# Kernel optimization log

Hardware: AMD Instinct MI355X
Metric: run time of the kernel (lower is better)

The kernel has to match this reference:

```python
import jax, jax.numpy as jnp
import numpy as np
from jax import lax

D = 1024      # hidden_dim
H = 1408      # moe_inter_dim
E = 8         # num_experts
K = 2         # topk
ROUTER_SCALE = 1.0


def setup_inputs() -> dict:
    key = jax.random.key(0)
    ks = jax.random.split(key, 16)
    s = 0.02
    inp = {
        "x": jax.random.normal(ks[0], (2, 2048, D), dtype=jnp.float32),
        "gate_w": jax.random.normal(ks[1], (E, D), dtype=jnp.float32) * s,
        "gate_b": jax.random.normal(ks[2], (E,), dtype=jnp.float32) * s,
        # stacked expert params; torch Linear weight [out,in] stored transposed as [in,out]
        "w1": jax.random.normal(ks[3], (E, D, H), dtype=jnp.float32) * s,
        "b1": jax.random.normal(ks[4], (E, H), dtype=jnp.float32) * s,
        "w3": jax.random.normal(ks[5], (E, D, H), dtype=jnp.float32) * s,
        "b3": jax.random.normal(ks[6], (E, H), dtype=jnp.float32) * s,
        "w2": jax.random.normal(ks[7], (E, H, D), dtype=jnp.float32) * s,
        "b2": jax.random.normal(ks[8], (E, D), dtype=jnp.float32) * s,
        # shared expert
        "sw1": jax.random.normal(ks[9], (D, H), dtype=jnp.float32) * s,
        "sb1": jax.random.normal(ks[10], (H,), dtype=jnp.float32) * s,
        "sw3": jax.random.normal(ks[11], (D, H), dtype=jnp.float32) * s,
        "sb3": jax.random.normal(ks[12], (H,), dtype=jnp.float32) * s,
        "sw2": jax.random.normal(ks[13], (H, D), dtype=jnp.float32) * s,
        "sb2": jax.random.normal(ks[14], (D,), dtype=jnp.float32) * s,
    }
    return inp


def _expert(x, w1, b1, w3, b3, w2, b2):
    # NOTE: source applies silu to the PRODUCT: w2(silu(w1(x) * w3(x)))
    h = jax.nn.silu((x @ w1 + b1) * (x @ w3 + b3))
    return h @ w2 + b2


def reference(x, gate_w, gate_b, w1, b1, w3, b3, w2, b2,
              sw1, sb1, sw3, sb3, sw2, sb2):
    shape = x.shape
    xf = x.reshape(-1, D)                      # [T, D]
    T = xf.shape[0]

    # Gate
    scores = jax.nn.softmax(xf @ gate_w.T, axis=-1)   # [T, E]
    biased = scores + gate_b
    _, idx = lax.top_k(biased, K)                     # [T, K] int32
    w = jnp.take_along_axis(scores, idx, axis=-1) * ROUTER_SCALE  # [T, K]

    # Dense routing-weight matrix (top-k indices are distinct per token)
    rw = jnp.zeros((T, E), dtype=xf.dtype).at[jnp.arange(T)[:, None], idx].add(w)

    # Stacked expert compute: [T, E, H] -> [T, E, D], combined by routing weight
    h = jax.nn.silu((jnp.einsum('td,edh->teh', xf, w1) + b1)
                    * (jnp.einsum('td,edh->teh', xf, w3) + b3))
    oe = jnp.einsum('teh,ehd->ted', h, w2) + b2
    y = jnp.einsum('te,ted->td', rw, oe)

    # Shared expert on all tokens
    z = _expert(xf, sw1, sb1, sw3, sb3, sw2, sb2)
    return (y + z).reshape(shape)
```

## Files before the change

kernel.cpp:

```cpp
#include <hip/hip_runtime.h>
#include <math.h>

#define DD 1024
#define HH 1408
#define NE 8

typedef __attribute__((ext_vector_type(8))) __bf16 bf16x8;
typedef __attribute__((ext_vector_type(4))) float f32x4;

__device__ __forceinline__ float bf2f(unsigned short u) {
  union { unsigned int i; float f; } v; v.i = ((unsigned int)u) << 16; return v.f;
}
__device__ __forceinline__ unsigned short f2bf(float f) {
  union { float f; unsigned int i; } v; v.f = f;
  unsigned int r = v.i + 0x7FFFu + ((v.i >> 16) & 1u);
  return (unsigned short)(r >> 16);
}
__device__ __forceinline__ float tof(float f) { return f; }
__device__ __forceinline__ float tof(unsigned short u) { return bf2f(u); }

__device__ __forceinline__ void cvt2(float a, float b, unsigned int* o) {
  asm("v_cvt_pk_bf16_f32 %0, %1, %2" : "=v"(*o) : "v"(a), "v"(b));
}

__device__ __forceinline__ void ld8cvt(const float* p, unsigned int* o) {
  float4 a = *(const float4*)p;
  float4 b = *(const float4*)(p + 4);
  cvt2(a.x, a.y, o + 0); cvt2(a.z, a.w, o + 1);
  cvt2(b.x, b.y, o + 2); cvt2(b.z, b.w, o + 3);
}

typedef unsigned int __attribute__((address_space(1))) gu32;
typedef unsigned int __attribute__((address_space(3))) lu32;
__device__ __forceinline__ void gl16(const unsigned short* g, unsigned short* l) {
  __builtin_amdgcn_global_load_lds((const gu32*)g, (lu32*)l, 16, 0, 0);
}

__global__ void sniff_kernel(const unsigned short* __restrict__ xw,
                             int* __restrict__ dflag) {
  __shared__ int cnt;
  if (threadIdx.x == 0) cnt = 0;
  __syncthreads();
  unsigned short v = xw[threadIdx.x];
  int e = (v >> 7) & 0xFF;
  if (e >= 100 && e <= 140) atomicAdd(&cnt, 1);
  __syncthreads();
  if (threadIdx.x == 0) dflag[0] = (cnt < 230) ? 1 : 0;
}

__global__ void cvtx_kernel(const void* __restrict__ x,
                            const int* __restrict__ dflag,
                            unsigned short* __restrict__ xb, int n8) {
  int i = blockIdx.x * blockDim.x + threadIdx.x;
  int st = gridDim.x * blockDim.x;
  if (dflag[0]) {
    const float* xs = (const float*)x;
    for (; i < n8; i += st) {
      unsigned int o[4];
      ld8cvt(xs + (size_t)i * 8, o);
      *(uint4*)(xb + (size_t)i * 8) = *(uint4*)o;
    }
  } else {
    const uint4* xs = (const uint4*)x;
    for (; i < n8; i += st) *(uint4*)(xb + (size_t)i * 8) = xs[i];
  }
}

__global__ void trans_kernel(const void* __restrict__ wmain,
                             const void* __restrict__ wsh,
                             const int* __restrict__ dflag,
                             unsigned short* __restrict__ out, int R, int C) {
  __shared__ float tile[32][33];
  const int mat = blockIdx.z;
  const int r0 = blockIdx.y << 5, c0 = blockIdx.x << 5;
  const int t = threadIdx.x;
  const int lr = t >> 3, lc = (t & 7) << 2;
  const size_t mbase = (size_t)mat * R * C;
  if (dflag[0]) {
    const float* src = (mat < NE) ? ((const float*)wmain + mbase) : (const float*)wsh;
    float4 v = *(const float4*)(src + (size_t)(r0 + lr) * C + c0 + lc);
    tile[lr][lc] = v.x; tile[lr][lc + 1] = v.y;
    tile[lr][lc + 2] = v.z; tile[lr][lc + 3] = v.w;
  } else {
    const unsigned short* src = (mat < NE) ? ((const unsigned short*)wmain + mbase)
                                           : (const unsigned short*)wsh;
    ushort4 v = *(const ushort4*)(src + (size_t)(r0 + lr) * C + c0 + lc);
    tile[lr][lc] = bf2f(v.x); tile[lr][lc + 1] = bf2f(v.y);
    tile[lr][lc + 2] = bf2f(v.z); tile[lr][lc + 3] = bf2f(v.w);
  }
  __syncthreads();
  const int oc = t >> 3;
  const int orr = (t & 7) << 2;
  unsigned int p0, p1;
  cvt2(tile[orr][oc], tile[orr + 1][oc], &p0);
  cvt2(tile[orr + 2][oc], tile[orr + 3][oc], &p1);
  uint2 pk; pk.x = p0; pk.y = p1;
  *(uint2*)(out + mbase + (size_t)(c0 + oc) * R + r0 + orr) = pk;
}

__global__ void cvtb_kernel(const void* b1, const void* b3, const void* b2,
                            const void* sb1, const void* sb3, const void* sb2,
                            const int* __restrict__ dflag,
                            float* __restrict__ bf1, float* __restrict__ bf3,
                            float* __restrict__ bf2o) {
  int i = blockIdx.x * blockDim.x + threadIdx.x;
  const int nh = (NE + 1) * HH, nd = (NE + 1) * DD;
  const bool f32 = dflag[0] != 0;
  auto get = [&](const void* pm, const void* ps, int idx, int per) -> float {
    int mat = idx / per, j = idx - mat * per;
    if (f32) return (mat < NE) ? ((const float*)pm)[(size_t)mat * per + j]
                               : ((const float*)ps)[j];
    return bf2f((mat < NE) ? ((const unsigned short*)pm)[(size_t)mat * per + j]
                           : ((const unsigned short*)ps)[j]);
  };
  if (i < nh) bf1[i] = get(b1, sb1, i, HH);
  else if (i < 2 * nh) bf3[i - nh] = get(b3, sb3, i - nh, HH);
  else if (i < 2 * nh + nd) bf2o[i - 2 * nh] = get(b2, sb2, i - 2 * nh, DD);
}

template <class T>
__device__ void gate_body(const T* __restrict__ x,
                          const T* __restrict__ gw,
                          const T* __restrict__ gb,
                          int* __restrict__ tok_eidx,
                          float* __restrict__ tok_w, int T_) {
  int t = (int)((blockIdx.x * blockDim.x + threadIdx.x) >> 6);
  int lane = threadIdx.x & 63;
  if (t >= T_) return;
  const T* xr = x + (size_t)t * DD;
  float acc[NE];
#pragma unroll
  for (int e = 0; e < NE; e++) acc[e] = 0.f;
  for (int i = lane; i < DD; i += 64) {
    float xv = tof(xr[i]);
#pragma unroll
    for (int e = 0; e < NE; e++) acc[e] += xv * tof(gw[e * DD + i]);
  }
#pragma unroll
  for (int off = 32; off > 0; off >>= 1) {
#pragma unroll
    for (int e = 0; e < NE; e++) acc[e] += __shfl_xor(acc[e], off);
  }
  if (lane == 0) {
    float mx = acc[0];
#pragma unroll
    for (int e = 1; e < NE; e++) mx = fmaxf(mx, acc[e]);
    float s = 0.f, sc[NE], bi[NE];
#pragma unroll
    for (int e = 0; e < NE; e++) { sc[e] = expf(acc[e] - mx); s += sc[e]; }
    float inv = 1.f / s;
#pragma unroll
    for (int e = 0; e < NE; e++) { sc[e] *= inv; bi[e] = sc[e] + tof(gb[e]); }
    int i1 = 0;
#pragma unroll
    for (int e = 1; e < NE; e++) if (bi[e] > bi[i1]) i1 = e;
    int i2 = (i1 == 0) ? 1 : 0;
#pragma unroll
    for (int e = 0; e < NE; e++) if (e != i1 && bi[e] > bi[i2]) i2 = e;
    tok_eidx[t * 2] = i1; tok_eidx[t * 2 + 1] = i2;
    tok_w[t * 2] = sc[i1]; tok_w[t * 2 + 1] = sc[i2];
  }
}

__global__ void gate_kernel(const void* x, const void* gw, const void* gb,
                            const int* __restrict__ dflag,
                            int* tok_eidx, float* tok_w, int T_) {
  if (dflag[0])
    gate_body<float>((const float*)x, (const float*)gw, (const float*)gb,
                     tok_eidx, tok_w, T_);
  else
    gate_body<unsigned short>((const unsigned short*)x, (const unsigned short*)gw,
                              (const unsigned short*)gb, tok_eidx, tok_w, T_);
}

__global__ void prep_kernel(const int* __restrict__ tok_eidx,
                            const float* __restrict__ tok_w,
                            int* __restrict__ meta,
                            int* __restrict__ rows_tok,
                            float* __restrict__ rows_wgt,
                            int* __restrict__ tok_pos,
                            int t0, int TS) {
  __shared__ int cnt[NE];
  __shared__ int off[NE];
  const int tid = threadIdx.x;
  if (tid < NE) cnt[tid] = 0;
  __syncthreads();
  const int n2 = TS * 2;
  const int* te = tok_eidx + (size_t)t0 * 2;
  const float* tw = tok_w + (size_t)t0 * 2;
  for (int i = tid; i < n2; i += (int)blockDim.x) atomicAdd(&cnt[te[i]], 1);
  __syncthreads();
  if (tid == 0) {
    int s = 0;
#pragma unroll
    for (int e = 0; e < NE; e++) { off[e] = s; meta[16 + e] = s; s += cnt[e]; }
    meta[16 + NE] = s;
  }
  __syncthreads();
  for (int i = tid; i < n2; i += (int)blockDim.x) {
    int pos = atomicAdd(&off[te[i]], 1);
    rows_tok[pos] = t0 + (i >> 1);
    rows_wgt[pos] = tw[i];
    tok_pos[(size_t)(t0 + (i >> 1)) * 2 + (i & 1)] = pos;
  }
}

__global__ void combine_kernel(const float4* __restrict__ r_out,
                               const int* __restrict__ tok_pos,
                               float4* __restrict__ out, int t0, int TS) {
  const int C4 = DD / 4;
  int i = blockIdx.x * blockDim.x + threadIdx.x;
  int n4 = TS * C4;
  int st = gridDim.x * blockDim.x;
  for (; i < n4; i += st) {
    int tl = i / C4, c = i - tl * C4;
    int t = t0 + tl;
    int p0 = tok_pos[t * 2], p1 = tok_pos[t * 2 + 1];
    float4 a = out[(size_t)t * C4 + c];
    float4 b = r_out[(size_t)p0 * C4 + c];
    float4 d = r_out[(size_t)p1 * C4 + c];
    a.x += b.x + d.x; a.y += b.y + d.y;
    a.z += b.z + d.z; a.w += b.w + d.w;
    out[(size_t)t * C4 + c] = a;
  }
}

__global__ __launch_bounds__(512, 2)
void ffn_up_kernel(const unsigned short* __restrict__ xb,
                   const unsigned short* __restrict__ wt1,
                   const unsigned short* __restrict__ wt3,
                   const float* __restrict__ bf1, const float* __restrict__ bf3,
                   const int* __restrict__ meta,
                   const int* __restrict__ rows_tok,
                   unsigned short* __restrict__ h_buf,
                   unsigned short* __restrict__ sh_buf,
                   int t0, int TS, int my) {
  const int NX = HH / 128;
  const int P = NX * (NE + 1);
  const int id = blockIdx.x;
  const int xcd = id & 7;
  const int rest = id >> 3;
  const int mtile = rest % my;
  const int chunk = rest / my;
  const int panel = chunk * 8 + xcd;
  if (panel >= P) return;
  const int z = panel / NX;
  const int n0 = (panel - z * NX) * 128;

  const bool shx = (z == NE);
  int g0, cnt;
  unsigned short* ho;
  if (shx) { g0 = 0; cnt = TS; ho = sh_buf; }
  else {
    g0 = meta[16 + z]; cnt = meta[17 + z] - g0;
    ho = h_buf + (size_t)g0 * HH;
  }
  if (mtile * 256 >= cnt) return;
  const unsigned short* wa = wt1 + (size_t)z * HH * DD;
  const unsigned short* wb = wt3 + (size_t)z * HH * DD;

  __shared__ alignas(16) unsigned short lds[3 * 16384];

  const int tid = threadIdx.x;
  const int lane = tid & 63, wid = tid >> 6;

  size_t aoff[2];
#pragma unroll
  for (int c = 0; c < 2; c++) {
    int g = c * 512 + tid;
    int r = g >> 2, s = g & 3;
    int m = mtile * 256 + r;
    int rr = (m < cnt) ? m : (cnt - 1);
    int srow = shx ? (t0 + rr) : rows_tok[g0 + rr];
    aoff[c] = (size_t)srow * DD + ((s ^ ((r >> 1) & 3)) << 3);
  }
  size_t boffs;
  {
    int rb = tid >> 2, sb = tid & 3;
    boffs = (size_t)(n0 + rb) * DD + ((sb ^ ((rb >> 1) & 3)) << 3);
  }
  const int wbase = wid * 512;

  const int ln15 = lane & 15;
  const int lg = lane >> 4;
  const int wr = (wid >> 1) << 6;
  const int wc = (wid & 1) << 6;

  f32x4 acc1[4][4], acc3[4][4];
#pragma unroll
  for (int a = 0; a < 4; a++)
#pragma unroll
    for (int b = 0; b < 4; b++) {
      acc1[a][b] = {0.f, 0.f, 0.f, 0.f};
      acc3[a][b] = {0.f, 0.f, 0.f, 0.f};
    }

  auto stage = [&](int buf, int k) {
    unsigned short* Lb = &lds[buf * 16384];
#pragma unroll
    for (int c = 0; c < 2; c++)
      gl16(xb + aoff[c] + k, Lb + c * 4096 + wbase);
    gl16(wa + boffs + k, Lb + 8192 + wbase);
    gl16(wb + boffs + k, Lb + 12288 + wbase);
  };

  const int NT = DD / 32;
  stage(0, 0);
  stage(1, 32);
  for (int t = 0; t < NT; ++t) {
    if (t + 1 < NT) asm volatile("s_waitcnt vmcnt(4)" ::: "memory");
    else            asm volatile("s_waitcnt vmcnt(0)" ::: "memory");
    asm volatile("s_barrier" ::: "memory");
    if (t + 2 < NT) stage((t + 2) % 3, (t + 2) * 32);
    const unsigned short* Lb = &lds[(t % 3) * 16384];
    bf16x8 af[4];
#pragma unroll
    for (int fm = 0; fm < 4; fm++) {
      int R = wr + fm * 16 + ln15;
      af[fm] = *(const bf16x8*)&Lb[R * 32 + ((lg ^ ((R >> 1) & 3)) << 3)];
    }
#pragma unroll
    for (int fn = 0; fn < 4; fn++) {
      int Rb = wc + fn * 16 + ln15;
      int o = Rb * 32 + ((lg ^ ((Rb >> 1) & 3)) << 3);
      bf16x8 b1v = *(const bf16x8*)&Lb[8192 + o];
      bf16x8 b3v = *(const bf16x8*)&Lb[12288 + o];
#pragma unroll
      for (int fm = 0; fm < 4; fm++) {
        acc1[fm][fn] = __builtin_amdgcn_mfma_f32_16x16x32_bf16(af[fm], b1v, acc1[fm][fn], 0, 0, 0);
        acc3[fm][fn] = __builtin_amdgcn_mfma_f32_16x16x32_bf16(af[fm], b3v, acc3[fm][fn], 0, 0, 0);
      }
    }
  }

  const int kq4 = lg << 2;
#pragma unroll
  for (int fm = 0; fm < 4; fm++) {
#pragma unroll
    for (int r = 0; r < 4; r++) {
      int m = mtile * 256 + wr + fm * 16 + kq4 + r;
      if (m < cnt) {
        unsigned short* orow = ho + (size_t)m * HH + n0;
#pragma unroll
        for (int fn = 0; fn < 4; fn++) {
          int nc = wc + fn * 16 + ln15;
          float g1 = acc1[fm][fn][r] + bf1[(size_t)z * HH + n0 + nc];
          float g3 = acc3[fm][fn][r] + bf3[(size_t)z * HH + n0 + nc];
          float u = g1 * g3;
          float hv = u * __builtin_amdgcn_rcpf(1.f + __expf(-u));
          orow[nc] = f2bf(hv);
        }
      }
    }
  }
}

__global__ __launch_bounds__(512, 2)
void ffn_down_kernel(const unsigned short* __restrict__ h_buf,
                     const unsigned short* __restrict__ sh_buf,
                     const unsigned short* __restrict__ wt2,
                     const float* __restrict__ bf2,
                     const int* __restrict__ meta,
                     const int* __restrict__ rows_tok,
                     const float* __restrict__ rows_wgt,
                     float* __restrict__ r_out,
                     float* __restrict__ out, int t0, int TS, int my) {
  const int NX = DD / 128;
  const int P = NX * (NE + 1);
  const int id = blockIdx.x;
  const int xcd = id & 7;
  const int rest = id >> 3;
  const int mtile = rest % my;
  const int chunk = rest / my;
  const int panel = chunk * 8 + xcd;
  if (panel >= P) return;
  const int z = panel / NX;
  const int n0 = (panel - z * NX) * 128;

  const bool shx = (z == NE);
  int g0, cnt;
  const unsigned short* hb;
  if (shx) { g0 = 0; cnt = TS; hb = sh_buf; }
  else {
    g0 = meta[16 + z]; cnt = meta[17 + z] - g0;
    hb = h_buf + (size_t)g0 * HH;
  }
  if (mtile * 256 >= cnt) return;
  const unsigned short* ws = wt2 + (size_t)z * DD * HH;

  __shared__ alignas(16) unsigned short lds[3 * 12288];

  const int tid = threadIdx.x;
  const int lane = tid & 63, wid = tid >> 6;

  size_t aoff[2];
#pragma unroll
  for (int c = 0; c < 2; c++) {
    int g = c * 512 + tid;
    int r = g >> 2, s = g & 3;
    int m = mtile * 256 + r;
    int rr = (m < cnt) ? m : (cnt - 1);
    aoff[c] = (size_t)rr * HH + ((s ^ ((r >> 1) & 3)) << 3);
  }
  size_t boffs;
  {
    int rb = tid >> 2, sb = tid & 3;
    boffs = (size_t)(n0 + rb) * HH + ((sb ^ ((rb >> 1) & 3)) << 3);
  }
  const int wbase = wid * 512;

  const int ln15 = lane & 15;
  const int lg = lane >> 4;
  const int wr = (wid >> 1) << 6;
  const int wc = (wid & 1) << 6;

  f32x4 acc[4][4];
#pragma unroll
  for (int a = 0; a < 4; a++)
#pragma unroll
    for (int b = 0; b < 4; b++) acc[a][b] = {0.f, 0.f, 0.f, 0.f};

  auto stage = [&](int buf, int k) {
    unsigned short* Lb = &lds[buf * 12288];
#pragma unroll
    for (int c = 0; c < 2; c++)
      gl16(hb + aoff[c] + k, Lb + c * 4096 + wbase);
    gl16(ws + boffs + k, Lb + 8192 + wbase);
  };

  const int NT = HH / 32;
  stage(0, 0);
  stage(1, 32);
  for (int t = 0; t < NT; ++t) {
    if (t + 1 < NT) asm volatile("s_waitcnt vmcnt(3)" ::: "memory");
    else            asm volatile("s_waitcnt vmcnt(0)" ::: "memory");
    asm volatile("s_barrier" ::: "memory");
    if (t + 2 < NT) stage((t + 2) % 3, (t + 2) * 32);
    const unsigned short* Lb = &lds[(t % 3) * 12288];
    bf16x8 af[4];
#pragma unroll
    for (int fm = 0; fm < 4; fm++) {
      int R = wr + fm * 16 + ln15;
      af[fm] = *(const bf16x8*)&Lb[R * 32 + ((lg ^ ((R >> 1) & 3)) << 3)];
    }
#pragma unroll
    for (int fn = 0; fn < 4; fn++) {
      int Rb = wc + fn * 16 + ln15;
      int o = Rb * 32 + ((lg ^ ((Rb >> 1) & 3)) << 3);
      bf16x8 bv = *(const bf16x8*)&Lb[8192 + o];
#pragma unroll
      for (int fm = 0; fm < 4; fm++)
        acc[fm][fn] = __builtin_amdgcn_mfma_f32_16x16x32_bf16(af[fm], bv, acc[fm][fn], 0, 0, 0);
    }
  }

  const int kq4 = lg << 2;
#pragma unroll
  for (int fm = 0; fm < 4; fm++) {
#pragma unroll
    for (int r4 = 0; r4 < 4; r4++) {
      int m = mtile * 256 + wr + fm * 16 + kq4 + r4;
      if (m < cnt) {
        float* orow;
        float wgt;
        if (shx) { orow = out + (size_t)(t0 + m) * DD + n0; wgt = 1.f; }
        else { orow = r_out + (size_t)(g0 + m) * DD + n0; wgt = rows_wgt[g0 + m]; }
#pragma unroll
        for (int fn = 0; fn < 4; fn++) {
          int nc = wc + fn * 16 + ln15;
          orow[nc] = wgt * (acc[fm][fn][r4] + bf2[(size_t)z * DD + n0 + nc]);
        }
      }
    }
  }
}

extern "C" void kernel_launch(void* const* d_in, const int* in_sizes, int n_in,
                              void* d_out, int out_size, void* d_ws, size_t ws_size,
                              hipStream_t stream) {
  const void* x   = d_in[0];
  const void* gw  = d_in[1];
  const void* gb  = d_in[2];
  const void* w1  = d_in[3];
  const void* b1  = d_in[4];
  const void* w3  = d_in[5];
  const void* b3  = d_in[6];
  const void* w2  = d_in[7];
  const void* b2  = d_in[8];
  const void* sw1 = d_in[9];
  const void* sb1 = d_in[10];
  const void* sw3 = d_in[11];
  const void* sb3 = d_in[12];
  const void* sw2 = d_in[13];
  const void* sb2 = d_in[14];

  const int T = in_sizes[0] / DD;
  (void)n_in; (void)out_size;

  const size_t WMAT = (size_t)(NE + 1) * HH * DD;

  auto need = [&](int S) -> size_t {
    int TS = T / S;
    size_t o = 0;
    auto pad = [&](size_t b) { o = (o + b + 255) & ~(size_t)255; };
    pad(256);
    pad(32 * sizeof(int));
    pad((size_t)T * 2 * sizeof(int));
    pad((size_t)T * 2 * sizeof(float));
    pad((size_t)T * 2 * sizeof(int));
    pad((size_t)T * DD * 2);
    pad(WMAT * 2);
    pad(WMAT * 2);
    pad(WMAT * 2);
    pad((size_t)(NE + 1) * HH * sizeof(float));
    pad((size_t)(NE + 1) * HH * sizeof(float));
    pad((size_t)(NE + 1) * DD * sizeof(float));
    pad((size_t)TS * 2 * sizeof(int));
    pad((size_t)TS * 2 * sizeof(float));
    pad((size_t)TS * 2 * HH * 2);
    pad((size_t)TS * HH * 2);
    pad((size_t)TS * 2 * DD * sizeof(float));
    return o;
  };
  int S = 32;
  {
    const int cand[6] = {1, 2, 4, 8, 16, 32};
    for (int ci = 0; ci < 6; ci++) {
      if (need(cand[ci]) <= ws_size) { S = cand[ci]; break; }
    }
  }
  const int TS = T / S;
  const int my = (TS + 255) / 256;

  char* w = (char*)d_ws;
  size_t off = 0;
  auto take = [&](size_t bytes) {
    char* p = w + off;
    off = (off + bytes + 255) & ~(size_t)255;
    return p;
  };
  int*   dflag    = (int*)  take(256);
  int*   meta     = (int*)  take(32 * sizeof(int));
  int*   tok_eidx = (int*)  take((size_t)T * 2 * sizeof(int));
  float* tok_w    = (float*)take((size_t)T * 2 * sizeof(float));
  int*   tok_pos  = (int*)  take((size_t)T * 2 * sizeof(int));
  unsigned short* xb  = (unsigned short*)take((size_t)T * DD * 2);
  unsigned short* wt1 = (unsigned short*)take(WMAT * 2);
  unsigned short* wt3 = (unsigned short*)take(WMAT * 2);
  unsigned short* wt2 = (unsigned short*)take(WMAT * 2);
  float* bf1 = (float*)take((size_t)(NE + 1) * HH * sizeof(float));
  float* bf3 = (float*)take((size_t)(NE + 1) * HH * sizeof(float));
  float* bf2 = (float*)take((size_t)(NE + 1) * DD * sizeof(float));
  int*   rows_tok = (int*)  take((size_t)TS * 2 * sizeof(int));
  float* rows_wgt = (float*)take((size_t)TS * 2 * sizeof(float));
  unsigned short* h_buf  = (unsigned short*)take((size_t)TS * 2 * HH * 2);
  unsigned short* sh_buf = (unsigned short*)take((size_t)TS * HH * 2);
  float* r_out = (float*)take((size_t)TS * 2 * DD * sizeof(float));

  sniff_kernel<<<1, 256, 0, stream>>>((const unsigned short*)x, dflag);

  cvtx_kernel<<<2048, 256, 0, stream>>>(x, dflag, xb, T * DD / 8);
  trans_kernel<<<dim3(HH / 32, DD / 32, NE + 1), 256, 0, stream>>>(w1, sw1, dflag, wt1, DD, HH);
  trans_kernel<<<dim3(HH / 32, DD / 32, NE + 1), 256, 0, stream>>>(w3, sw3, dflag, wt3, DD, HH);
  trans_kernel<<<dim3(DD / 32, HH / 32, NE + 1), 256, 0, stream>>>(w2, sw2, dflag, wt2, HH, DD);
  {
    int nb = (2 * (NE + 1) * HH + (NE + 1) * DD + 255) / 256;
    cvtb_kernel<<<nb, 256, 0, stream>>>(b1, b3, b2, sb1, sb3, sb2, dflag, bf1, bf3, bf2);
  }

  gate_kernel<<<(T + 3) / 4, 256, 0, stream>>>(x, gw, gb, dflag, tok_eidx, tok_w, T);

  const int upP = (HH / 128) * (NE + 1);
  const int dnP = (DD / 128) * (NE + 1);
  const int upGrid = 8 * ((upP + 7) / 8) * my;
  const int dnGrid = 8 * ((dnP + 7) / 8) * my;

  for (int s = 0; s < S; s++) {
    const int t0 = s * TS;
    prep_kernel<<<1, 1024, 0, stream>>>(tok_eidx, tok_w, meta, rows_tok, rows_wgt,
                                        tok_pos, t0, TS);
    ffn_up_kernel<<<upGrid, 512, 0, stream>>>(
        xb, wt1, wt3, bf1, bf3, meta, rows_tok, h_buf, sh_buf, t0, TS, my);
    ffn_down_kernel<<<dnGrid, 512, 0, stream>>>(
        h_buf, sh_buf, wt2, bf2, meta, rows_tok, rows_wgt, r_out,
        (float*)d_out, t0, TS, my);
    combine_kernel<<<1024, 256, 0, stream>>>((const float4*)r_out, tok_pos,
                                             (float4*)d_out, t0, TS);
  }
}
```

Baseline: 440.1 us.

## Shrink FFN GEMM M-tile to 128 and use double buffering for higher occupancy

Both expert GEMM kernels drop the M tile from 256 to 128 rows, cut per-wave accumulators in half, and move from a three-stage LDS pipeline to two-stage double buffering with a full vmcnt(0) wait and __syncthreads each step. Launch bounds rise from 2 to 4 blocks per CU so more waves can hide latency and small expert groups waste less padding. In exchange, weight tiles are reloaded for twice as many M tiles and prefetch depth shrinks, which may expose memory latency.

New measurement: 425.6 us. 3.3% less time.

```diff
diff --git a/kernel.cpp b/kernel.cpp
--- a/kernel.cpp
+++ b/kernel.cpp
@@ -225,7 +225,7 @@
   }
 }
 
-__global__ __launch_bounds__(512, 2)
+__global__ __launch_bounds__(512, 4)
 void ffn_up_kernel(const unsigned short* __restrict__ xb,
                    const unsigned short* __restrict__ wt1,
                    const unsigned short* __restrict__ wt3,
@@ -255,40 +255,35 @@
     g0 = meta[16 + z]; cnt = meta[17 + z] - g0;
     ho = h_buf + (size_t)g0 * HH;
   }
-  if (mtile * 256 >= cnt) return;
+  if (mtile * 128 >= cnt) return;
   const unsigned short* wa = wt1 + (size_t)z * HH * DD;
   const unsigned short* wb = wt3 + (size_t)z * HH * DD;
 
-  __shared__ alignas(16) unsigned short lds[3 * 16384];
+  __shared__ alignas(16) unsigned short lds[2 * 12288];
 
   const int tid = threadIdx.x;
   const int lane = tid & 63, wid = tid >> 6;
 
-  size_t aoff[2];
-#pragma unroll
-  for (int c = 0; c < 2; c++) {
-    int g = c * 512 + tid;
-    int r = g >> 2, s = g & 3;
-    int m = mtile * 256 + r;
+  const int grow = tid >> 2, gslot = tid & 3;
+  const int gcol = (gslot ^ ((grow >> 1) & 3)) << 3;
+  size_t aoffs;
+  {
+    int m = mtile * 128 + grow;
     int rr = (m < cnt) ? m : (cnt - 1);
     int srow = shx ? (t0 + rr) : rows_tok[g0 + rr];
-    aoff[c] = (size_t)srow * DD + ((s ^ ((r >> 1) & 3)) << 3);
-  }
-  size_t boffs;
-  {
-    int rb = tid >> 2, sb = tid & 3;
-    boffs = (size_t)(n0 + rb) * DD + ((sb ^ ((rb >> 1) & 3)) << 3);
-  }
+    aoffs = (size_t)srow * DD + gcol;
+  }
+  const size_t boffs = (size_t)(n0 + grow) * DD + gcol;
   const int wbase = wid * 512;
 
   const int ln15 = lane & 15;
   const int lg = lane >> 4;
-  const int wr = (wid >> 1) << 6;
+  const int wr = (wid >> 1) << 5;
   const int wc = (wid & 1) << 6;
 
-  f32x4 acc1[4][4], acc3[4][4];
-#pragma unroll
-  for (int a = 0; a < 4; a++)
+  f32x4 acc1[2][4], acc3[2][4];
+#pragma unroll
+  for (int a = 0; a < 2; a++)
 #pragma unroll
     for (int b = 0; b < 4; b++) {
       acc1[a][b] = {0.f, 0.f, 0.f, 0.f};
@@ -296,26 +291,22 @@
     }
 
   auto stage = [&](int buf, int k) {
-    unsigned short* Lb = &lds[buf * 16384];
-#pragma unroll
-    for (int c = 0; c < 2; c++)
-      gl16(xb + aoff[c] + k, Lb + c * 4096 + wbase);
-    gl16(wa + boffs + k, Lb + 8192 + wbase);
-    gl16(wb + boffs + k, Lb + 12288 + wbase);
+    unsigned short* Lb = &lds[buf * 12288];
+    gl16(xb + aoffs + k, Lb + wbase);
+    gl16(wa + boffs + k, Lb + 4096 + wbase);
+    gl16(wb + boffs + k, Lb + 8192 + wbase);
   };
 
   const int NT = DD / 32;
   stage(0, 0);
-  stage(1, 32);
   for (int t = 0; t < NT; ++t) {
-    if (t + 1 < NT) asm volatile("s_waitcnt vmcnt(4)" ::: "memory");
-    else            asm volatile("s_waitcnt vmcnt(0)" ::: "memory");
-    asm volatile("s_barrier" ::: "memory");
-    if (t + 2 < NT) stage((t + 2) % 3, (t + 2) * 32);
-    const unsigned short* Lb = &lds[(t % 3) * 16384];
-    bf16x8 af[4];
-#pragma unroll
-    for (int fm = 0; fm < 4; fm++) {
+    asm volatile("s_waitcnt vmcnt(0)" ::: "memory");
+    __syncthreads();
+    if (t + 1 < NT) stage((t + 1) & 1, (t + 1) * 32);
+    const unsigned short* Lb = &lds[(t & 1) * 12288];
+    bf16x8 af[2];
+#pragma unroll
+    for (int fm = 0; fm < 2; fm++) {
       int R = wr + fm * 16 + ln15;
       af[fm] = *(const bf16x8*)&Lb[R * 32 + ((lg ^ ((R >> 1) & 3)) << 3)];
     }
@@ -323,10 +314,10 @@
     for (int fn = 0; fn < 4; fn++) {
       int Rb = wc + fn * 16 + ln15;
       int o = Rb * 32 + ((lg ^ ((Rb >> 1) & 3)) << 3);
-      bf16x8 b1v = *(const bf16x8*)&Lb[8192 + o];
-      bf16x8 b3v = *(const bf16x8*)&Lb[12288 + o];
-#pragma unroll
-      for (int fm = 0; fm < 4; fm++) {
+      bf16x8 b1v = *(const bf16x8*)&Lb[4096 + o];
+      bf16x8 b3v = *(const bf16x8*)&Lb[8192 + o];
+#pragma unroll
+      for (int fm = 0; fm < 2; fm++) {
         acc1[fm][fn] = __builtin_amdgcn_mfma_f32_16x16x32_bf16(af[fm], b1v, acc1[fm][fn], 0, 0, 0);
         acc3[fm][fn] = __builtin_amdgcn_mfma_f32_16x16x32_bf16(af[fm], b3v, acc3[fm][fn], 0, 0, 0);
       }
@@ -335,10 +326,10 @@
 
   const int kq4 = lg << 2;
 #pragma unroll
-  for (int fm = 0; fm < 4; fm++) {
+  for (int fm = 0; fm < 2; fm++) {
 #pragma unroll
     for (int r = 0; r < 4; r++) {
-      int m = mtile * 256 + wr + fm * 16 + kq4 + r;
+      int m = mtile * 128 + wr + fm * 16 + kq4 + r;
       if (m < cnt) {
         unsigned short* orow = ho + (size_t)m * HH + n0;
 #pragma unroll
@@ -355,7 +346,7 @@
   }
 }
 
-__global__ __launch_bounds__(512, 2)
+__global__ __launch_bounds__(512, 4)
 void ffn_down_kernel(const unsigned short* __restrict__ h_buf,
                      const unsigned short* __restrict__ sh_buf,
                      const unsigned short* __restrict__ wt2,
@@ -385,61 +376,52 @@
     g0 = meta[16 + z]; cnt = meta[17 + z] - g0;
     hb = h_buf + (size_t)g0 * HH;
   }
-  if (mtile * 256 >= cnt) return;
+  if (mtile * 128 >= cnt) return;
   const unsigned short* ws = wt2 + (size_t)z * DD * HH;
 
-  __shared__ alignas(16) unsigned short lds[3 * 12288];
+  __shared__ alignas(16) unsigned short lds[2 * 8192];
 
   const int tid = threadIdx.x;
   const int lane = tid & 63, wid = tid >> 6;
 
-  size_t aoff[2];
-#pragma unroll
-  for (int c = 0; c < 2; c++) {
-    int g = c * 512 + tid;
-    int r = g >> 2, s = g & 3;
-    int m = mtile * 256 + r;
+  const int grow = tid >> 2, gslot = tid & 3;
+  const int gcol = (gslot ^ ((grow >> 1) & 3)) << 3;
+  size_t aoffs;
+  {
+    int m = mtile * 128 + grow;
     int rr = (m < cnt) ? m : (cnt - 1);
-    aoff[c] = (size_t)rr * HH + ((s ^ ((r >> 1) & 3)) << 3);
-  }
-  size_t boffs;
-  {
-    int rb = tid >> 2, sb = tid & 3;
-    boffs = (size_t)(n0 + rb) * HH + ((sb ^ ((rb >> 1) & 3)) << 3);
-  }
+    aoffs = (size_t)rr * HH + gcol;
+  }
+  const size_t boffs = (size_t)(n0 + grow) * HH + gcol;
   const int wbase = wid * 512;
 
   const int ln15 = lane & 15;
   const int lg = lane >> 4;
-  const int wr = (wid >> 1) << 6;
+  const int wr = (wid >> 1) << 5;
   const int wc = (wid & 1) << 6;
 
-  f32x4 acc[4][4];
-#pragma unroll
-  for (int a = 0; a < 4; a++)
+  f32x4 acc[2][4];
+#pragma unroll
+  for (int a = 0; a < 2; a++)
 #pragma unroll
     for (int b = 0; b < 4; b++) acc[a][b] = {0.f, 0.f, 0.f, 0.f};
 
   auto stage = [&](int buf, int k) {
-    unsigned short* Lb = &lds[buf * 12288];
-#pragma unroll
-    for (int c = 0; c < 2; c++)
-      gl16(hb + aoff[c] + k, Lb + c * 4096 + wbase);
-    gl16(ws + boffs + k, Lb + 8192 + wbase);
+    unsigned short* Lb = &lds[buf * 8192];
+    gl16(hb + aoffs + k, Lb + wbase);
+    gl16(ws + boffs + k, Lb + 4096 + wbase);
   };
 
   const int NT = HH / 32;
   stage(0, 0);
-  stage(1, 32);
   for (int t = 0; t < NT; ++t) {
-    if (t + 1 < NT) asm volatile("s_waitcnt vmcnt(3)" ::: "memory");
-    else            asm volatile("s_waitcnt vmcnt(0)" ::: "memory");
-    asm volatile("s_barrier" ::: "memory");
-    if (t + 2 < NT) stage((t + 2) % 3, (t + 2) * 32);
-    const unsigned short* Lb = &lds[(t % 3) * 12288];
-    bf16x8 af[4];
-#pragma unroll
-    for (int fm = 0; fm < 4; fm++) {
+    asm volatile("s_waitcnt vmcnt(0)" ::: "memory");
+    __syncthreads();
+    if (t + 1 < NT) stage((t + 1) & 1, (t + 1) * 32);
+    const unsigned short* Lb = &lds[(t & 1) * 8192];
+    bf16x8 af[2];
+#pragma unroll
+    for (int fm = 0; fm < 2; fm++) {
       int R = wr + fm * 16 + ln15;
       af[fm] = *(const bf16x8*)&Lb[R * 32 + ((lg ^ ((R >> 1) & 3)) << 3)];
     }
@@ -447,19 +429,19 @@
     for (int fn = 0; fn < 4; fn++) {
       int Rb = wc + fn * 16 + ln15;
       int o = Rb * 32 + ((lg ^ ((Rb >> 1) & 3)) << 3);
-      bf16x8 bv = *(const bf16x8*)&Lb[8192 + o];
-#pragma unroll
-      for (int fm = 0; fm < 4; fm++)
+      bf16x8 bv = *(const bf16x8*)&Lb[4096 + o];
+#pragma unroll
+      for (int fm = 0; fm < 2; fm++)
         acc[fm][fn] = __builtin_amdgcn_mfma_f32_16x16x32_bf16(af[fm], bv, acc[fm][fn], 0, 0, 0);
     }
   }
 
   const int kq4 = lg << 2;
 #pragma unroll
-  for (int fm = 0; fm < 4; fm++) {
+  for (int fm = 0; fm < 2; fm++) {
 #pragma unroll
     for (int r4 = 0; r4 < 4; r4++) {
-      int m = mtile * 256 + wr + fm * 16 + kq4 + r4;
+      int m = mtile * 128 + wr + fm * 16 + kq4 + r4;
       if (m < cnt) {
         float* orow;
         float wgt;
@@ -530,7 +512,7 @@
     }
   }
   const int TS = T / S;
-  const int my = (TS + 255) / 256;
+  const int my = (TS + 127) / 128;
 
   char* w = (char*)d_ws;
   size_t off = 0;
```
